# Optimization experiments

Hardware: AMD Instinct MI355X
Metric: run time of the kernel (lower is better)

## Reference

```python
import jax, jax.numpy as jnp
import numpy as np

N_NODES = 50000


def _gcn_norm(edge_index, n):
    # improved=True: self-loops with weight 2.0, sym normalization
    src, dst = edge_index[0], edge_index[1]
    loop = jnp.arange(n, dtype=src.dtype)
    src_f = jnp.concatenate([src, loop])
    dst_f = jnp.concatenate([dst, loop])
    ew = jnp.concatenate([jnp.ones(src.shape[0], jnp.float32),
                          jnp.full((n,), 2.0, jnp.float32)])
    deg = jax.ops.segment_sum(ew, dst_f, num_segments=n)
    dinv = jnp.where(deg > 0, jax.lax.rsqrt(deg), 0.0)
    norm = dinv[src_f] * ew * dinv[dst_f]
    return src_f, dst_f, norm


def _gcn_conv(x, W, b, src_f, dst_f, norm, n):
    h = x @ W  # [N, C_out]
    msg = h[src_f] * norm[:, None]  # gather + scale, [E+N, C_out]
    out = jax.ops.segment_sum(msg, dst_f, num_segments=n)  # scatter-add
    return out + b


def setup_inputs() -> dict:
    key = jax.random.key(0)
    ks = jax.random.split(key, 12)
    n, f_in, h, labels, e = N_NODES, 256, 128, 128, 800000
    s = 1.0 / np.sqrt(f_in)
    sh = 1.0 / np.sqrt(h)
    return {
        "x": jax.random.normal(ks[0], (n, f_in), jnp.float32),
        "edge_index": jax.random.randint(ks[1], (2, e), 0, n, jnp.int64),
        "W1": jax.random.uniform(ks[2], (f_in, h), jnp.float32, -s, s),
        "b1": jnp.zeros((h,), jnp.float32),
        "W2": jax.random.uniform(ks[3], (h, h), jnp.float32, -sh, sh),
        "b2": jnp.zeros((h,), jnp.float32),
        "We": jax.random.uniform(ks[4], (h, h), jnp.float32, -sh, sh),
        "be": jnp.zeros((h,), jnp.float32),
        "Wf": jax.random.uniform(ks[5], (h, labels), jnp.float32, -sh, sh),
        "bf": jax.random.uniform(ks[6], (labels,), jnp.float32, -sh, sh),
    }


def reference(x, edge_index, W1, b1, W2, b2, We, be, Wf, bf):
    n = x.shape[0]
    src_f, dst_f, norm = _gcn_norm(edge_index, n)
    h = jax.nn.relu(_gcn_conv(x, W1, b1, src_f, dst_f, norm, n))
    h = jax.nn.relu(_gcn_conv(h, W2, b2, src_f, dst_f, norm, n))
    h = _gcn_conv(h, We, be, src_f, dst_f, norm, n)
    return jax.nn.sigmoid(h @ Wf + bf)
```

## Files before the change

kernel.cpp:

```cpp
#include <hip/hip_runtime.h>
#include <stdint.h>

static constexpr int NN  = 50000;
static constexpr int EE  = 800000;
static constexpr int FIN = 256;
static constexpr int HID = 128;
static constexpr int SZ_LOG = 8;
static constexpr int NBUCK  = (NN + 255) >> SZ_LOG;
static constexpr int CH     = 2048;
static constexpr int NCBLK  = (EE + CH - 1) / CH;

typedef __attribute__((ext_vector_type(8))) short  short8;
typedef __attribute__((ext_vector_type(8))) __bf16 bf16x8;
typedef __attribute__((ext_vector_type(4))) float  f32x4;
typedef uint16_t u16;

__device__ __forceinline__ u16 f2bf(float f) {
  union { float f; uint32_t u; } v; v.f = f;
  return (u16)((v.u + 0x7fffu + ((v.u >> 16) & 1u)) >> 16);
}
__device__ __forceinline__ float bflo(uint32_t u) {
  union { uint32_t u; float f; } v; v.u = u << 16; return v.f;
}
__device__ __forceinline__ float bfhi(uint32_t u) {
  union { uint32_t u; float f; } v; v.u = u & 0xffff0000u; return v.f;
}

__global__ void k_zero(int* p, int n) {
  int i = blockIdx.x * 256 + threadIdx.x;
  if (i < n) p[i] = 0;
}

__global__ __launch_bounds__(256) void k_bhist(const int* __restrict__ dst, int* __restrict__ bcnt, int e) {
  __shared__ int lc[NBUCK];
  int tid = threadIdx.x;
  for (int i = tid; i < NBUCK; i += 256) lc[i] = 0;
  __syncthreads();
  int base = blockIdx.x * CH;
#pragma unroll
  for (int j = 0; j < 8; ++j) {
    int i = base + j * 256 + tid;
    if (i < e) atomicAdd(&lc[dst[i] >> SZ_LOG], 1);
  }
  __syncthreads();
  for (int i = tid; i < NBUCK; i += 256) if (lc[i]) atomicAdd(&bcnt[i], lc[i]);
}

__global__ __launch_bounds__(256) void k_bscan(const int* __restrict__ bcnt, int* __restrict__ boff,
                                               int* __restrict__ bcur, int* __restrict__ off) {
  __shared__ int buf[256];
  int tid = threadIdx.x;
  int v = (tid < NBUCK) ? bcnt[tid] : 0;
  buf[tid] = v;
  __syncthreads();
  for (int o = 1; o < 256; o <<= 1) {
    int t = (tid >= o) ? buf[tid - o] : 0;
    __syncthreads();
    buf[tid] += t;
    __syncthreads();
  }
  int ex = buf[tid] - v;
  if (tid < NBUCK) { boff[tid] = ex; bcur[tid] = ex; }
  if (tid == NBUCK - 1) boff[NBUCK] = ex + v;
  if (tid == 0) off[NN] = EE;
}

__global__ __launch_bounds__(256) void k_bscatter(const int* __restrict__ src, const int* __restrict__ dst,
                                                  int* __restrict__ bcur, int2* __restrict__ ebuck, int e) {
  __shared__ int lc[NBUCK];
  __shared__ int lb[NBUCK];
  int tid = threadIdx.x;
  for (int i = tid; i < NBUCK; i += 256) lc[i] = 0;
  __syncthreads();
  int base = blockIdx.x * CH;
  int sj[8], dj[8], rj[8];
#pragma unroll
  for (int j = 0; j < 8; ++j) {
    int i = base + j * 256 + tid;
    if (i < e) {
      sj[j] = src[i]; dj[j] = dst[i];
      rj[j] = atomicAdd(&lc[dj[j] >> SZ_LOG], 1);
    }
  }
  __syncthreads();
  for (int i = tid; i < NBUCK; i += 256) { int c = lc[i]; if (c) lb[i] = atomicAdd(&bcur[i], c); }
  __syncthreads();
#pragma unroll
  for (int j = 0; j < 8; ++j) {
    int i = base + j * 256 + tid;
    if (i < e) ebuck[lb[dj[j] >> SZ_LOG] + rj[j]] = make_int2(sj[j], dj[j]);
  }
}

__global__ __launch_bounds__(256) void k_ncount(const int2* __restrict__ ebuck, const int* __restrict__ boff,
                                                int* __restrict__ off, float* __restrict__ dinv) {
  __shared__ int nc[256];
  __shared__ int sc[256];
  int b = blockIdx.x, tid = threadIdx.x;
  nc[tid] = 0;
  __syncthreads();
  int j0 = boff[b], j1 = boff[b + 1];
  for (int j = j0 + tid; j < j1; j += 256) atomicAdd(&nc[ebuck[j].y & 255], 1);
  __syncthreads();
  int v = nc[tid];
  sc[tid] = v;
  __syncthreads();
  for (int o = 1; o < 256; o <<= 1) {
    int t = (tid >= o) ? sc[tid - o] : 0;
    __syncthreads();
    sc[tid] += t;
    __syncthreads();
  }
  int node = (b << SZ_LOG) + tid;
  if (node < NN) {
    off[node]  = j0 + sc[tid] - v;
    dinv[node] = rsqrtf((float)v + 2.0f);
  }
}

__global__ __launch_bounds__(256) void k_fill2(const int2* __restrict__ ebuck, const int* __restrict__ boff,
                                               const int* __restrict__ off, const float* __restrict__ dinv,
                                               int2* __restrict__ edges) {
  __shared__ int   lcur[256];
  __shared__ float ldv[256];
  int b = blockIdx.x, tid = threadIdx.x;
  int node = (b << SZ_LOG) + tid;
  lcur[tid] = (node < NN) ? off[node]  : 0;
  ldv[tid]  = (node < NN) ? dinv[node] : 0.f;
  __syncthreads();
  int j0 = boff[b], j1 = boff[b + 1];
  for (int j = j0 + tid; j < j1; j += 256) {
    int2 e = ebuck[j];
    int loc = e.y & 255;
    int pos = atomicAdd(&lcur[loc], 1);
    edges[pos] = make_int2(e.x, __float_as_int(dinv[e.x] * ldv[loc]));
  }
}

__global__ void k_wconv_all(const float* __restrict__ W1, const float* __restrict__ W2,
                            const float* __restrict__ We, const float* __restrict__ Wf,
                            u16* __restrict__ T1, u16* __restrict__ T2,
                            u16* __restrict__ T3, u16* __restrict__ T4) {
  int i = blockIdx.x * 256 + threadIdx.x;
  const float* W; u16* o;
  if (i < 32768)      { W = W1; o = T1; }
  else if (i < 49152) { W = W2; o = T2; i -= 32768; }
  else if (i < 65536) { W = We; o = T3; i -= 49152; }
  else                { W = Wf; o = T4; i -= 65536; }
  int k = i >> 7, c = i & 127;
  o[(size_t)((k >> 5) * 128 + c) * 32 + (k & 31)] = f2bf(W[i]);
}

template<int AFLOAT, int EPI>
__global__ __launch_bounds__(256) void k_gemm(const float* __restrict__ Af, const u16* __restrict__ Ah,
                                              const u16* __restrict__ Wt, const float* __restrict__ bias,
                                              u16* __restrict__ gout, float* __restrict__ fout,
                                              int M, int K) {
  __shared__ u16 Ash[64 * 40];
  __shared__ u16 Bsh[128 * 40];
  const int tid  = threadIdx.x;
  const int lane = tid & 63;
  const int w    = tid >> 6;
  const int row0 = blockIdx.x * 64;
  f32x4 acc[8];
#pragma unroll
  for (int t = 0; t < 8; ++t) acc[t] = (f32x4){0.f, 0.f, 0.f, 0.f};

  const int nk = K >> 5;
  const int r = tid >> 2, kg = tid & 3;
  const int grow_a = row0 + r;
  for (int kb = 0; kb < nk; ++kb) {
    {
      int k0 = kb * 32 + kg * 8;
      alignas(16) u16 v[8];
      if (grow_a < M) {
        if (AFLOAT) {
          const float* p = Af + (size_t)grow_a * K + k0;
          float4 x0 = *(const float4*)(p);
          float4 x1 = *(const float4*)(p + 4);
          v[0] = f2bf(x0.x); v[1] = f2bf(x0.y); v[2] = f2bf(x0.z); v[3] = f2bf(x0.w);
          v[4] = f2bf(x1.x); v[5] = f2bf(x1.y); v[6] = f2bf(x1.z); v[7] = f2bf(x1.w);
        } else {
          *(uint4*)v = *(const uint4*)(Ah + (size_t)grow_a * K + k0);
        }
      } else {
#pragma unroll
        for (int i = 0; i < 8; ++i) v[i] = 0;
      }
      *(uint4*)&Ash[r * 40 + kg * 8] = *(const uint4*)v;
    }
    {
      const u16* wsrc = Wt + (size_t)kb * 4096;
#pragma unroll
      for (int j = 0; j < 2; ++j) {
        int chunk = tid * 2 + j;
        int rowb = chunk >> 2, kk = (chunk & 3) << 3;
        *(uint4*)&Bsh[rowb * 40 + kk] = *(const uint4*)(wsrc + chunk * 8);
      }
    }
    __syncthreads();
    {
      const int rl = lane & 15, kq = lane >> 4;
      short8 af = *(const short8*)&Ash[(w * 16 + rl) * 40 + kq * 8];
#pragma unroll
      for (int t = 0; t < 8; ++t) {
        short8 bf = *(const short8*)&Bsh[(t * 16 + rl) * 40 + kq * 8];
        acc[t] = __builtin_amdgcn_mfma_f32_16x16x32_bf16(
            __builtin_bit_cast(bf16x8, af), __builtin_bit_cast(bf16x8, bf), acc[t], 0, 0, 0);
      }
    }
    __syncthreads();
  }
  const int rl = lane & 15, rq = lane >> 4;
#pragma unroll
  for (int t = 0; t < 8; ++t) {
    int col = t * 16 + rl;
#pragma unroll
    for (int i = 0; i < 4; ++i) {
      int grow = row0 + w * 16 + rq * 4 + i;
      if (grow < M) {
        if (EPI == 0) {
          gout[(size_t)grow * HID + col] = f2bf(acc[t][i]);
        } else {
          float vv = acc[t][i] + bias[col];
          fout[(size_t)grow * HID + col] = 1.0f / (1.0f + __expf(-vv));
        }
      }
    }
  }
}

template<int RELU>
__global__ __launch_bounds__(256) void k_agg(const u16* __restrict__ h, u16* __restrict__ g,
                                             const float* __restrict__ bias, const float* __restrict__ dinv,
                                             const int* __restrict__ off, const int2* __restrict__ edges,
                                             int n) {
  int wave = blockIdx.x * 4 + (threadIdx.x >> 6);
  int lane = threadIdx.x & 63;
  if (wave >= n) return;
  const int d  = wave;
  const int gr = lane >> 4;
  const int t  = lane & 15;
  const int c  = t << 3;
  float a[8];
#pragma unroll
  for (int i = 0; i < 8; ++i) a[i] = 0.f;

  int j  = off[d] + gr;
  const int j1 = off[d + 1];
  for (; j + 4 < j1; j += 8) {
    int2 eA = edges[j], eB = edges[j + 4];
    uint4 vA = *(const uint4*)(h + (size_t)eA.x * HID + c);
    uint4 vB = *(const uint4*)(h + (size_t)eB.x * HID + c);
    float wA = __int_as_float(eA.y), wB = __int_as_float(eB.y);
    a[0] += wA * bflo(vA.x); a[1] += wA * bfhi(vA.x);
    a[2] += wA * bflo(vA.y); a[3] += wA * bfhi(vA.y);
    a[4] += wA * bflo(vA.z); a[5] += wA * bfhi(vA.z);
    a[6] += wA * bflo(vA.w); a[7] += wA * bfhi(vA.w);
    a[0] += wB * bflo(vB.x); a[1] += wB * bfhi(vB.x);
    a[2] += wB * bflo(vB.y); a[3] += wB * bfhi(vB.y);
    a[4] += wB * bflo(vB.z); a[5] += wB * bfhi(vB.z);
    a[6] += wB * bflo(vB.w); a[7] += wB * bfhi(vB.w);
  }
  for (; j < j1; j += 4) {
    int2 eA = edges[j];
    uint4 vA = *(const uint4*)(h + (size_t)eA.x * HID + c);
    float wA = __int_as_float(eA.y);
    a[0] += wA * bflo(vA.x); a[1] += wA * bfhi(vA.x);
    a[2] += wA * bflo(vA.y); a[3] += wA * bfhi(vA.y);
    a[4] += wA * bflo(vA.z); a[5] += wA * bfhi(vA.z);
    a[6] += wA * bflo(vA.w); a[7] += wA * bfhi(vA.w);
  }
#pragma unroll
  for (int i = 0; i < 8; ++i) {
    a[i] += __shfl_xor(a[i], 16);
    a[i] += __shfl_xor(a[i], 32);
  }
  float di = dinv[d];
  float sl = 2.0f * di * di;
  uint4 sv = *(const uint4*)(h + (size_t)d * HID + c);
  const float4 bv0 = *(const float4*)(bias + c);
  const float4 bv1 = *(const float4*)(bias + c + 4);
  a[0] += sl * bflo(sv.x) + bv0.x; a[1] += sl * bfhi(sv.x) + bv0.y;
  a[2] += sl * bflo(sv.y) + bv0.z; a[3] += sl * bfhi(sv.y) + bv0.w;
  a[4] += sl * bflo(sv.z) + bv1.x; a[5] += sl * bfhi(sv.z) + bv1.y;
  a[6] += sl * bflo(sv.w) + bv1.z; a[7] += sl * bfhi(sv.w) + bv1.w;
  if (RELU) {
#pragma unroll
    for (int i = 0; i < 8; ++i) a[i] = fmaxf(a[i], 0.f);
  }
  if (gr == 0) {
    uint4 o;
    o.x = (uint32_t)f2bf(a[0]) | ((uint32_t)f2bf(a[1]) << 16);
    o.y = (uint32_t)f2bf(a[2]) | ((uint32_t)f2bf(a[3]) << 16);
    o.z = (uint32_t)f2bf(a[4]) | ((uint32_t)f2bf(a[5]) << 16);
    o.w = (uint32_t)f2bf(a[6]) | ((uint32_t)f2bf(a[7]) << 16);
    *(uint4*)(g + (size_t)d * HID + c) = o;
  }
}

extern "C" void kernel_launch(void* const* d_in, const int* in_sizes, int n_in,
                              void* d_out, int out_size, void* d_ws, size_t ws_size,
                              hipStream_t stream) {
  const float* x   = (const float*)d_in[0];
  const int*   ei  = (const int*)d_in[1];
  const float* W1  = (const float*)d_in[2];
  const float* b1  = (const float*)d_in[3];
  const float* W2  = (const float*)d_in[4];
  const float* b2  = (const float*)d_in[5];
  const float* We  = (const float*)d_in[6];
  const float* be  = (const float*)d_in[7];
  const float* Wf  = (const float*)d_in[8];
  const float* bfv = (const float*)d_in[9];
  float* out = (float*)d_out;

  const int* src = ei;
  const int* dst = ei + EE;

  char* p = (char*)d_ws;
  auto take = [&](size_t bytes) { char* r = p; p += (bytes + 255) & ~(size_t)255; return r; };
  int*   bcnt  = (int*)take((size_t)NBUCK * 4);
  int*   boff  = (int*)take((size_t)(NBUCK + 1) * 4);
  int*   bcur  = (int*)take((size_t)NBUCK * 4);
  int*   off   = (int*)take((size_t)(NN + 1) * 4);
  float* dinv  = (float*)take((size_t)NN * 4);
  int2*  edges = (int2*)take((size_t)EE * 8);
  u16*   hA    = (u16*)take((size_t)NN * HID * 2);
  u16*   hB    = (u16*)take((size_t)NN * HID * 2);
  u16*   Wt1   = (u16*)take((size_t)FIN * HID * 2);
  u16*   Wt2   = (u16*)take((size_t)HID * HID * 2);
  u16*   Wt3   = (u16*)take((size_t)HID * HID * 2);
  u16*   Wt4   = (u16*)take((size_t)HID * HID * 2);
  int2*  ebuck = (int2*)hB;

  k_zero<<<1, 256, 0, stream>>>(bcnt, NBUCK);
  k_bhist<<<NCBLK, 256, 0, stream>>>(dst, bcnt, EE);
  k_bscan<<<1, 256, 0, stream>>>(bcnt, boff, bcur, off);
  k_bscatter<<<NCBLK, 256, 0, stream>>>(src, dst, bcur, ebuck, EE);
  k_ncount<<<NBUCK, 256, 0, stream>>>(ebuck, boff, off, dinv);
  k_fill2<<<NBUCK, 256, 0, stream>>>(ebuck, boff, off, dinv, edges);

  k_wconv_all<<<(81920 + 255) / 256, 256, 0, stream>>>(W1, W2, We, Wf, Wt1, Wt2, Wt3, Wt4);

  const int gemm_grid = (NN + 63) / 64;
  const int agg_grid  = (NN + 3) / 4;

  k_gemm<1, 0><<<gemm_grid, 256, 0, stream>>>(x, nullptr, Wt1, nullptr, hA, nullptr, NN, FIN);
  k_agg<1><<<agg_grid, 256, 0, stream>>>(hA, hB, b1, dinv, off, edges, NN);
  k_gemm<0, 0><<<gemm_grid, 256, 0, stream>>>(nullptr, hB, Wt2, nullptr, hA, nullptr, NN, HID);
  k_agg<1><<<agg_grid, 256, 0, stream>>>(hA, hB, b2, dinv, off, edges, NN);
  k_gemm<0, 0><<<gemm_grid, 256, 0, stream>>>(nullptr, hB, Wt3, nullptr, hA, nullptr, NN, HID);
  k_agg<0><<<agg_grid, 256, 0, stream>>>(hA, hB, be, dinv, off, edges, NN);
  k_gemm<0, 1><<<gemm_grid, 256, 0, stream>>>(nullptr, hB, Wt4, bfv, nullptr, out, NN, HID);
}
```

Before: 304.0 us.

## Double-buffer GEMM shared tiles, unroll aggregation gathers by four, use memset

The GEMM kernel now uses two shared-memory buffers and prefetches the next K-tile's A and B data into registers while MFMAs run on the current tile, so each iteration needs one barrier instead of two. The aggregation loop gets a 4-way unrolled path so more independent neighbor gathers are in flight per lane. The zeroing kernel is replaced by hipMemsetAsync. Costs are more registers and twice the LDS per GEMM block, plus a redundant scalar store to Bsh before each vector store.

```diff
diff --git a/kernel.cpp b/kernel.cpp
--- a/kernel.cpp
+++ b/kernel.cpp
@@ -25,10 +25,11 @@
 __device__ __forceinline__ float bfhi(uint32_t u) {
   union { uint32_t u; float f; } v; v.u = u & 0xffff0000u; return v.f;
 }
-
-__global__ void k_zero(int* p, int n) {
-  int i = blockIdx.x * 256 + threadIdx.x;
-  if (i < n) p[i] = 0;
+__device__ __forceinline__ void accum8(float a[8], uint4 v, float wn) {
+  a[0] += wn * bflo(v.x); a[1] += wn * bfhi(v.x);
+  a[2] += wn * bflo(v.y); a[3] += wn * bfhi(v.y);
+  a[4] += wn * bflo(v.z); a[5] += wn * bfhi(v.z);
+  a[6] += wn * bflo(v.w); a[7] += wn * bfhi(v.w);
 }
 
 __global__ __launch_bounds__(256) void k_bhist(const int* __restrict__ dst, int* __restrict__ bcnt, int e) {
@@ -156,8 +157,8 @@
                                               const u16* __restrict__ Wt, const float* __restrict__ bias,
                                               u16* __restrict__ gout, float* __restrict__ fout,
                                               int M, int K) {
-  __shared__ u16 Ash[64 * 40];
-  __shared__ u16 Bsh[128 * 40];
+  __shared__ u16 Ash[2][64 * 40];
+  __shared__ u16 Bsh[2][128 * 40];
   const int tid  = threadIdx.x;
   const int lane = tid & 63;
   const int w    = tid >> 6;
@@ -169,49 +170,77 @@
   const int nk = K >> 5;
   const int r = tid >> 2, kg = tid & 3;
   const int grow_a = row0 + r;
+  const bool arow_ok = (grow_a < M);
+
+  float  fa[8];
+  uint4  ua;
+  uint4  vb[2];
+
+  auto loadA = [&](int kb) {
+    int k0 = kb * 32 + kg * 8;
+    if (AFLOAT) {
+      if (arow_ok) {
+        const float* p = Af + (size_t)grow_a * K + k0;
+        float4 x0 = *(const float4*)(p);
+        float4 x1 = *(const float4*)(p + 4);
+        fa[0] = x0.x; fa[1] = x0.y; fa[2] = x0.z; fa[3] = x0.w;
+        fa[4] = x1.x; fa[5] = x1.y; fa[6] = x1.z; fa[7] = x1.w;
+      } else {
+#pragma unroll
+        for (int i = 0; i < 8; ++i) fa[i] = 0.f;
+      }
+    } else {
+      if (arow_ok) ua = *(const uint4*)(Ah + (size_t)grow_a * K + kb * 32 + kg * 8);
+      else ua = make_uint4(0, 0, 0, 0);
+    }
+  };
+  auto loadB = [&](int kb) {
+    const u16* wsrc = Wt + (size_t)kb * 4096;
+#pragma unroll
+    for (int j = 0; j < 2; ++j) vb[j] = *(const uint4*)(wsrc + (tid * 2 + j) * 8);
+  };
+  auto storeA = [&](int buf) {
+    if (AFLOAT) {
+      alignas(16) u16 v[8];
+#pragma unroll
+      for (int i = 0; i < 8; ++i) v[i] = f2bf(fa[i]);
+      *(uint4*)&Ash[buf][r * 40 + kg * 8] = *(const uint4*)v;
+    } else {
+      *(uint4*)&Ash[buf][r * 40 + kg * 8] = ua;
+    }
+  };
+  auto storeB = [&](int buf) {
+#pragma unroll
+    for (int j = 0; j < 2; ++j) {
+      int chunk = tid * 2 + j;
+      Bsh[buf][(chunk >> 2) * 40 + ((chunk & 3) << 3)] = 0;
+      *(uint4*)&Bsh[buf][(chunk >> 2) * 40 + ((chunk & 3) << 3)] = vb[j];
+    }
+  };
+
+  loadA(0); loadB(0);
+  storeA(0); storeB(0);
+  __syncthreads();
+
+  const int rl = lane & 15, kq = lane >> 4;
   for (int kb = 0; kb < nk; ++kb) {
-    {
-      int k0 = kb * 32 + kg * 8;
-      alignas(16) u16 v[8];
-      if (grow_a < M) {
-        if (AFLOAT) {
-          const float* p = Af + (size_t)grow_a * K + k0;
-          float4 x0 = *(const float4*)(p);
-          float4 x1 = *(const float4*)(p + 4);
-          v[0] = f2bf(x0.x); v[1] = f2bf(x0.y); v[2] = f2bf(x0.z); v[3] = f2bf(x0.w);
-          v[4] = f2bf(x1.x); v[5] = f2bf(x1.y); v[6] = f2bf(x1.z); v[7] = f2bf(x1.w);
-        } else {
-          *(uint4*)v = *(const uint4*)(Ah + (size_t)grow_a * K + k0);
-        }
-      } else {
-#pragma unroll
-        for (int i = 0; i < 8; ++i) v[i] = 0;
-      }
-      *(uint4*)&Ash[r * 40 + kg * 8] = *(const uint4*)v;
-    }
-    {
-      const u16* wsrc = Wt + (size_t)kb * 4096;
-#pragma unroll
-      for (int j = 0; j < 2; ++j) {
-        int chunk = tid * 2 + j;
-        int rowb = chunk >> 2, kk = (chunk & 3) << 3;
-        *(uint4*)&Bsh[rowb * 40 + kk] = *(const uint4*)(wsrc + chunk * 8);
-      }
-    }
-    __syncthreads();
-    {
-      const int rl = lane & 15, kq = lane >> 4;
-      short8 af = *(const short8*)&Ash[(w * 16 + rl) * 40 + kq * 8];
-#pragma unroll
-      for (int t = 0; t < 8; ++t) {
-        short8 bf = *(const short8*)&Bsh[(t * 16 + rl) * 40 + kq * 8];
-        acc[t] = __builtin_amdgcn_mfma_f32_16x16x32_bf16(
-            __builtin_bit_cast(bf16x8, af), __builtin_bit_cast(bf16x8, bf), acc[t], 0, 0, 0);
-      }
-    }
-    __syncthreads();
-  }
-  const int rl = lane & 15, rq = lane >> 4;
+    const int cur = kb & 1;
+    const bool more = (kb + 1 < nk);
+    if (more) { loadA(kb + 1); loadB(kb + 1); }
+    short8 af = *(const short8*)&Ash[cur][(w * 16 + rl) * 40 + kq * 8];
+#pragma unroll
+    for (int t = 0; t < 8; ++t) {
+      short8 bf = *(const short8*)&Bsh[cur][(t * 16 + rl) * 40 + kq * 8];
+      acc[t] = __builtin_amdgcn_mfma_f32_16x16x32_bf16(
+          __builtin_bit_cast(bf16x8, af), __builtin_bit_cast(bf16x8, bf), acc[t], 0, 0, 0);
+    }
+    if (more) {
+      storeA(cur ^ 1); storeB(cur ^ 1);
+      __syncthreads();
+    }
+  }
+
+  const int rq = lane >> 4;
 #pragma unroll
   for (int t = 0; t < 8; ++t) {
     int col = t * 16 + rl;
@@ -248,28 +277,28 @@
 
   int j  = off[d] + gr;
   const int j1 = off[d + 1];
+  for (; j + 12 < j1; j += 16) {
+    int2 e0 = edges[j], e1 = edges[j + 4], e2 = edges[j + 8], e3 = edges[j + 12];
+    uint4 v0 = *(const uint4*)(h + (size_t)e0.x * HID + c);
+    uint4 v1 = *(const uint4*)(h + (size_t)e1.x * HID + c);
+    uint4 v2 = *(const uint4*)(h + (size_t)e2.x * HID + c);
+    uint4 v3 = *(const uint4*)(h + (size_t)e3.x * HID + c);
+    accum8(a, v0, __int_as_float(e0.y));
+    accum8(a, v1, __int_as_float(e1.y));
+    accum8(a, v2, __int_as_float(e2.y));
+    accum8(a, v3, __int_as_float(e3.y));
+  }
   for (; j + 4 < j1; j += 8) {
-    int2 eA = edges[j], eB = edges[j + 4];
-    uint4 vA = *(const uint4*)(h + (size_t)eA.x * HID + c);
-    uint4 vB = *(const uint4*)(h + (size_t)eB.x * HID + c);
-    float wA = __int_as_float(eA.y), wB = __int_as_float(eB.y);
-    a[0] += wA * bflo(vA.x); a[1] += wA * bfhi(vA.x);
-    a[2] += wA * bflo(vA.y); a[3] += wA * bfhi(vA.y);
-    a[4] += wA * bflo(vA.z); a[5] += wA * bfhi(vA.z);
-    a[6] += wA * bflo(vA.w); a[7] += wA * bfhi(vA.w);
-    a[0] += wB * bflo(vB.x); a[1] += wB * bfhi(vB.x);
-    a[2] += wB * bflo(vB.y); a[3] += wB * bfhi(vB.y);
-    a[4] += wB * bflo(vB.z); a[5] += wB * bfhi(vB.z);
-    a[6] += wB * bflo(vB.w); a[7] += wB * bfhi(vB.w);
+    int2 e0 = edges[j], e1 = edges[j + 4];
+    uint4 v0 = *(const uint4*)(h + (size_t)e0.x * HID + c);
+    uint4 v1 = *(const uint4*)(h + (size_t)e1.x * HID + c);
+    accum8(a, v0, __int_as_float(e0.y));
+    accum8(a, v1, __int_as_float(e1.y));
   }
   for (; j < j1; j += 4) {
-    int2 eA = edges[j];
-    uint4 vA = *(const uint4*)(h + (size_t)eA.x * HID + c);
-    float wA = __int_as_float(eA.y);
-    a[0] += wA * bflo(vA.x); a[1] += wA * bfhi(vA.x);
-    a[2] += wA * bflo(vA.y); a[3] += wA * bfhi(vA.y);
-    a[4] += wA * bflo(vA.z); a[5] += wA * bfhi(vA.z);
-    a[6] += wA * bflo(vA.w); a[7] += wA * bfhi(vA.w);
+    int2 e0 = edges[j];
+    uint4 v0 = *(const uint4*)(h + (size_t)e0.x * HID + c);
+    accum8(a, v0, __int_as_float(e0.y));
   }
 #pragma unroll
   for (int i = 0; i < 8; ++i) {
@@ -333,7 +362,7 @@
   u16*   Wt4   = (u16*)take((size_t)HID * HID * 2);
   int2*  ebuck = (int2*)hB;
 
-  k_zero<<<1, 256, 0, stream>>>(bcnt, NBUCK);
+  hipMemsetAsync(bcnt, 0, (size_t)NBUCK * 4, stream);
   k_bhist<<<NCBLK, 256, 0, stream>>>(dst, bcnt, EE);
   k_bscan<<<1, 256, 0, stream>>>(bcnt, boff, bcur, off);
   k_bscatter<<<NCBLK, 256, 0, stream>>>(src, dst, bcur, ebuck, EE);
```

After: 331.7 us. 1.09x slower.

## Factor symmetric normalization into GEMM epilogue and shrink edge records to int

Applied to the files above, without the earlier changes.

Moves the source-side dinv scaling into the GEMM epilogue (h' = dinv*h) and applies the destination dinv once after aggregation. Edge weights no longer need to be stored, so edge records shrink from int2 to a single int. The bucket pass packs src and local dst into one int. The aggregation loop is unrolled to four gathers per step, and the zero kernel becomes a memset. This halves edge-index traffic and removes per-edge multiplies, at the cost of a src<<8 packing that assumes node ids fit in 24 bits and slightly different bf16 rounding.

```diff
diff --git a/kernel.cpp b/kernel.cpp
--- a/kernel.cpp
+++ b/kernel.cpp
@@ -25,10 +25,11 @@
 __device__ __forceinline__ float bfhi(uint32_t u) {
   union { uint32_t u; float f; } v; v.u = u & 0xffff0000u; return v.f;
 }
-
-__global__ void k_zero(int* p, int n) {
-  int i = blockIdx.x * 256 + threadIdx.x;
-  if (i < n) p[i] = 0;
+__device__ __forceinline__ void add8(float a[8], uint4 v) {
+  a[0] += bflo(v.x); a[1] += bfhi(v.x);
+  a[2] += bflo(v.y); a[3] += bfhi(v.y);
+  a[4] += bflo(v.z); a[5] += bfhi(v.z);
+  a[6] += bflo(v.w); a[7] += bfhi(v.w);
 }
 
 __global__ __launch_bounds__(256) void k_bhist(const int* __restrict__ dst, int* __restrict__ bcnt, int e) {
@@ -66,7 +67,7 @@
 }
 
 __global__ __launch_bounds__(256) void k_bscatter(const int* __restrict__ src, const int* __restrict__ dst,
-                                                  int* __restrict__ bcur, int2* __restrict__ ebuck, int e) {
+                                                  int* __restrict__ bcur, int* __restrict__ ebuck, int e) {
   __shared__ int lc[NBUCK];
   __shared__ int lb[NBUCK];
   int tid = threadIdx.x;
@@ -88,11 +89,11 @@
 #pragma unroll
   for (int j = 0; j < 8; ++j) {
     int i = base + j * 256 + tid;
-    if (i < e) ebuck[lb[dj[j] >> SZ_LOG] + rj[j]] = make_int2(sj[j], dj[j]);
-  }
-}
-
-__global__ __launch_bounds__(256) void k_ncount(const int2* __restrict__ ebuck, const int* __restrict__ boff,
+    if (i < e) ebuck[lb[dj[j] >> SZ_LOG] + rj[j]] = (sj[j] << 8) | (dj[j] & 255);
+  }
+}
+
+__global__ __launch_bounds__(256) void k_ncount(const int* __restrict__ ebuck, const int* __restrict__ boff,
                                                 int* __restrict__ off, float* __restrict__ dinv) {
   __shared__ int nc[256];
   __shared__ int sc[256];
@@ -100,7 +101,7 @@
   nc[tid] = 0;
   __syncthreads();
   int j0 = boff[b], j1 = boff[b + 1];
-  for (int j = j0 + tid; j < j1; j += 256) atomicAdd(&nc[ebuck[j].y & 255], 1);
+  for (int j = j0 + tid; j < j1; j += 256) atomicAdd(&nc[ebuck[j] & 255], 1);
   __syncthreads();
   int v = nc[tid];
   sc[tid] = v;
@@ -118,22 +119,18 @@
   }
 }
 
-__global__ __launch_bounds__(256) void k_fill2(const int2* __restrict__ ebuck, const int* __restrict__ boff,
-                                               const int* __restrict__ off, const float* __restrict__ dinv,
-                                               int2* __restrict__ edges) {
-  __shared__ int   lcur[256];
-  __shared__ float ldv[256];
+__global__ __launch_bounds__(256) void k_fill2(const int* __restrict__ ebuck, const int* __restrict__ boff,
+                                               const int* __restrict__ off, int* __restrict__ edges) {
+  __shared__ int lcur[256];
   int b = blockIdx.x, tid = threadIdx.x;
   int node = (b << SZ_LOG) + tid;
-  lcur[tid] = (node < NN) ? off[node]  : 0;
-  ldv[tid]  = (node < NN) ? dinv[node] : 0.f;
+  lcur[tid] = (node < NN) ? off[node] : 0;
   __syncthreads();
   int j0 = boff[b], j1 = boff[b + 1];
   for (int j = j0 + tid; j < j1; j += 256) {
-    int2 e = ebuck[j];
-    int loc = e.y & 255;
-    int pos = atomicAdd(&lcur[loc], 1);
-    edges[pos] = make_int2(e.x, __float_as_int(dinv[e.x] * ldv[loc]));
+    int e = ebuck[j];
+    int pos = atomicAdd(&lcur[e & 255], 1);
+    edges[pos] = e >> 8;
   }
 }
 
@@ -154,6 +151,7 @@
 template<int AFLOAT, int EPI>
 __global__ __launch_bounds__(256) void k_gemm(const float* __restrict__ Af, const u16* __restrict__ Ah,
                                               const u16* __restrict__ Wt, const float* __restrict__ bias,
+                                              const float* __restrict__ dinv,
                                               u16* __restrict__ gout, float* __restrict__ fout,
                                               int M, int K) {
   __shared__ u16 Ash[64 * 40];
@@ -213,14 +211,15 @@
   }
   const int rl = lane & 15, rq = lane >> 4;
 #pragma unroll
-  for (int t = 0; t < 8; ++t) {
-    int col = t * 16 + rl;
-#pragma unroll
-    for (int i = 0; i < 4; ++i) {
-      int grow = row0 + w * 16 + rq * 4 + i;
-      if (grow < M) {
+  for (int i = 0; i < 4; ++i) {
+    int grow = row0 + w * 16 + rq * 4 + i;
+    if (grow < M) {
+      float dv = (EPI == 0) ? dinv[grow] : 0.f;
+#pragma unroll
+      for (int t = 0; t < 8; ++t) {
+        int col = t * 16 + rl;
         if (EPI == 0) {
-          gout[(size_t)grow * HID + col] = f2bf(acc[t][i]);
+          gout[(size_t)grow * HID + col] = f2bf(dv * acc[t][i]);
         } else {
           float vv = acc[t][i] + bias[col];
           fout[(size_t)grow * HID + col] = 1.0f / (1.0f + __expf(-vv));
@@ -233,7 +232,7 @@
 template<int RELU>
 __global__ __launch_bounds__(256) void k_agg(const u16* __restrict__ h, u16* __restrict__ g,
                                              const float* __restrict__ bias, const float* __restrict__ dinv,
-                                             const int* __restrict__ off, const int2* __restrict__ edges,
+                                             const int* __restrict__ off, const int* __restrict__ edges,
                                              int n) {
   int wave = blockIdx.x * 4 + (threadIdx.x >> 6);
   int lane = threadIdx.x & 63;
@@ -248,28 +247,23 @@
 
   int j  = off[d] + gr;
   const int j1 = off[d + 1];
+  for (; j + 12 < j1; j += 16) {
+    int s0 = edges[j], s1 = edges[j + 4], s2 = edges[j + 8], s3 = edges[j + 12];
+    uint4 v0 = *(const uint4*)(h + (size_t)s0 * HID + c);
+    uint4 v1 = *(const uint4*)(h + (size_t)s1 * HID + c);
+    uint4 v2 = *(const uint4*)(h + (size_t)s2 * HID + c);
+    uint4 v3 = *(const uint4*)(h + (size_t)s3 * HID + c);
+    add8(a, v0); add8(a, v1); add8(a, v2); add8(a, v3);
+  }
   for (; j + 4 < j1; j += 8) {
-    int2 eA = edges[j], eB = edges[j + 4];
-    uint4 vA = *(const uint4*)(h + (size_t)eA.x * HID + c);
-    uint4 vB = *(const uint4*)(h + (size_t)eB.x * HID + c);
-    float wA = __int_as_float(eA.y), wB = __int_as_float(eB.y);
-    a[0] += wA * bflo(vA.x); a[1] += wA * bfhi(vA.x);
-    a[2] += wA * bflo(vA.y); a[3] += wA * bfhi(vA.y);
-    a[4] += wA * bflo(vA.z); a[5] += wA * bfhi(vA.z);
-    a[6] += wA * bflo(vA.w); a[7] += wA * bfhi(vA.w);
-    a[0] += wB * bflo(vB.x); a[1] += wB * bfhi(vB.x);
-    a[2] += wB * bflo(vB.y); a[3] += wB * bfhi(vB.y);
-    a[4] += wB * bflo(vB.z); a[5] += wB * bfhi(vB.z);
-    a[6] += wB * bflo(vB.w); a[7] += wB * bfhi(vB.w);
+    int s0 = edges[j], s1 = edges[j + 4];
+    uint4 v0 = *(const uint4*)(h + (size_t)s0 * HID + c);
+    uint4 v1 = *(const uint4*)(h + (size_t)s1 * HID + c);
+    add8(a, v0); add8(a, v1);
   }
   for (; j < j1; j += 4) {
-    int2 eA = edges[j];
-    uint4 vA = *(const uint4*)(h + (size_t)eA.x * HID + c);
-    float wA = __int_as_float(eA.y);
-    a[0] += wA * bflo(vA.x); a[1] += wA * bfhi(vA.x);
-    a[2] += wA * bflo(vA.y); a[3] += wA * bfhi(vA.y);
-    a[4] += wA * bflo(vA.z); a[5] += wA * bfhi(vA.z);
-    a[6] += wA * bflo(vA.w); a[7] += wA * bfhi(vA.w);
+    uint4 v0 = *(const uint4*)(h + (size_t)edges[j] * HID + c);
+    add8(a, v0);
   }
 #pragma unroll
   for (int i = 0; i < 8; ++i) {
@@ -277,14 +271,17 @@
     a[i] += __shfl_xor(a[i], 32);
   }
   float di = dinv[d];
-  float sl = 2.0f * di * di;
   uint4 sv = *(const uint4*)(h + (size_t)d * HID + c);
   const float4 bv0 = *(const float4*)(bias + c);
   const float4 bv1 = *(const float4*)(bias + c + 4);
-  a[0] += sl * bflo(sv.x) + bv0.x; a[1] += sl * bfhi(sv.x) + bv0.y;
-  a[2] += sl * bflo(sv.y) + bv0.z; a[3] += sl * bfhi(sv.y) + bv0.w;
-  a[4] += sl * bflo(sv.z) + bv1.x; a[5] += sl * bfhi(sv.z) + bv1.y;
-  a[6] += sl * bflo(sv.w) + bv1.z; a[7] += sl * bfhi(sv.w) + bv1.w;
+  a[0] = bv0.x + di * (a[0] + 2.f * bflo(sv.x));
+  a[1] = bv0.y + di * (a[1] + 2.f * bfhi(sv.x));
+  a[2] = bv0.z + di * (a[2] + 2.f * bflo(sv.y));
+  a[3] = bv0.w + di * (a[3] + 2.f * bfhi(sv.y));
+  a[4] = bv1.x + di * (a[4] + 2.f * bflo(sv.z));
+  a[5] = bv1.y + di * (a[5] + 2.f * bfhi(sv.z));
+  a[6] = bv1.z + di * (a[6] + 2.f * bflo(sv.w));
+  a[7] = bv1.w + di * (a[7] + 2.f * bfhi(sv.w));
   if (RELU) {
 #pragma unroll
     for (int i = 0; i < 8; ++i) a[i] = fmaxf(a[i], 0.f);
@@ -324,32 +321,32 @@
   int*   bcur  = (int*)take((size_t)NBUCK * 4);
   int*   off   = (int*)take((size_t)(NN + 1) * 4);
   float* dinv  = (float*)take((size_t)NN * 4);
-  int2*  edges = (int2*)take((size_t)EE * 8);
+  int*   edges = (int*)take((size_t)EE * 4);
   u16*   hA    = (u16*)take((size_t)NN * HID * 2);
   u16*   hB    = (u16*)take((size_t)NN * HID * 2);
   u16*   Wt1   = (u16*)take((size_t)FIN * HID * 2);
   u16*   Wt2   = (u16*)take((size_t)HID * HID * 2);
   u16*   Wt3   = (u16*)take((size_t)HID * HID * 2);
   u16*   Wt4   = (u16*)take((size_t)HID * HID * 2);
-  int2*  ebuck = (int2*)hB;
-
-  k_zero<<<1, 256, 0, stream>>>(bcnt, NBUCK);
+  int*   ebuck = (int*)hB;
+
+  hipMemsetAsync(bcnt, 0, (size_t)NBUCK * 4, stream);
   k_bhist<<<NCBLK, 256, 0, stream>>>(dst, bcnt, EE);
   k_bscan<<<1, 256, 0, stream>>>(bcnt, boff, bcur, off);
   k_bscatter<<<NCBLK, 256, 0, stream>>>(src, dst, bcur, ebuck, EE);
   k_ncount<<<NBUCK, 256, 0, stream>>>(ebuck, boff, off, dinv);
-  k_fill2<<<NBUCK, 256, 0, stream>>>(ebuck, boff, off, dinv, edges);
+  k_fill2<<<NBUCK, 256, 0, stream>>>(ebuck, boff, off, edges);
 
   k_wconv_all<<<(81920 + 255) / 256, 256, 0, stream>>>(W1, W2, We, Wf, Wt1, Wt2, Wt3, Wt4);
 
   const int gemm_grid = (NN + 63) / 64;
   const int agg_grid  = (NN + 3) / 4;
 
-  k_gemm<1, 0><<<gemm_grid, 256, 0, stream>>>(x, nullptr, Wt1, nullptr, hA, nullptr, NN, FIN);
+  k_gemm<1, 0><<<gemm_grid, 256, 0, stream>>>(x, nullptr, Wt1, nullptr, dinv, hA, nullptr, NN, FIN);
   k_agg<1><<<agg_grid, 256, 0, stream>>>(hA, hB, b1, dinv, off, edges, NN);
-  k_gemm<0, 0><<<gemm_grid, 256, 0, stream>>>(nullptr, hB, Wt2, nullptr, hA, nullptr, NN, HID);
+  k_gemm<0, 0><<<gemm_grid, 256, 0, stream>>>(nullptr, hB, Wt2, nullptr, dinv, hA, nullptr, NN, HID);
   k_agg<1><<<agg_grid, 256, 0, stream>>>(hA, hB, b2, dinv, off, edges, NN);
-  k_gemm<0, 0><<<gemm_grid, 256, 0, stream>>>(nullptr, hB, Wt3, nullptr, hA, nullptr, NN, HID);
+  k_gemm<0, 0><<<gemm_grid, 256, 0, stream>>>(nullptr, hB, Wt3, nullptr, dinv, hA, nullptr, NN, HID);
   k_agg<0><<<agg_grid, 256, 0, stream>>>(hA, hB, be, dinv, off, edges, NN);
-  k_gemm<0, 1><<<gemm_grid, 256, 0, stream>>>(nullptr, hB, Wt4, bfv, nullptr, out, NN, HID);
-}
+  k_gemm<0, 1><<<gemm_grid, 256, 0, stream>>>(nullptr, hB, Wt4, bfv, dinv, nullptr, out, NN, HID);
+}
```

After: 293.7 us. -3.4%, faster.
